# Kernel optimization log

Hardware: AMD Instinct MI355X
Metric: run time of the kernel (lower is better)

The kernel has to match this reference:

```python
import jax, jax.numpy as jnp
import numpy as np

B, S, D, H = 64, 32, 1024, 1024


def setup_inputs() -> dict:
    key = jax.random.key(0)
    ks = jax.random.split(key, 12)
    sd = 1.0 / np.sqrt(D)
    sh = 1.0 / np.sqrt(H)
    return {
        "local_descs_t": jax.random.normal(ks[0], (B, S, D), jnp.float32),
        "local_descs_rot": jax.random.normal(ks[1], (B, S, D), jnp.float32),
        "scene_w": jax.random.normal(ks[2], (2 * D,), jnp.float32) * sd,
        "scene_b": jax.random.normal(ks[3], (1,), jnp.float32),
        "Wt1": jax.random.normal(ks[4], (S, D, H), jnp.float32) * sd,
        "bt1": jax.random.normal(ks[5], (S, H), jnp.float32) * 0.01,
        "Wt2": jax.random.normal(ks[6], (S, H, 3), jnp.float32) * sh,
        "bt2": jax.random.normal(ks[7], (S, 3), jnp.float32) * 0.01,
        "Wr1": jax.random.normal(ks[8], (S, D, H), jnp.float32) * sd,
        "br1": jax.random.normal(ks[9], (S, H), jnp.float32) * 0.01,
        "Wr2": jax.random.normal(ks[10], (S, H, 4), jnp.float32) * sh,
        "br2": jax.random.normal(ks[11], (S, 4), jnp.float32) * 0.01,
    }


def _pose_head(g, idx, W1, b1, W2, b2):
    # g: [B, D]; gather per-sample expert weights and run 2-layer MLP (GELU, exact erf as in F.gelu)
    h = jax.nn.gelu(jnp.einsum("bd,bdh->bh", g, W1[idx]) + b1[idx], approximate=False)
    return jnp.einsum("bh,bho->bo", h, W2[idx]) + b2[idx]


def reference(local_descs_t, local_descs_rot, scene_w, scene_b,
              Wt1, bt1, Wt2, bt2, Wr1, br1, Wr2, br2):
    # scene classification: Linear(2D -> 1) over concat descriptors, log-softmax over scenes
    logits = jnp.einsum("bsd,d->bs",
                        jnp.concatenate([local_descs_t, local_descs_rot], axis=2),
                        scene_w) + scene_b  # [B, S]
    scene_log_distr = jax.nn.log_softmax(logits, axis=1)
    idx = jnp.argmax(scene_log_distr, axis=1)  # top-1 scene per sample, [B]
    # select the chosen scene's descriptor (equivalent to one-hot mask * descs, summed over scenes)
    global_desc_t = jnp.take_along_axis(local_descs_t, idx[:, None, None], axis=1)[:, 0]    # [B, D]
    global_desc_rot = jnp.take_along_axis(local_descs_rot, idx[:, None, None], axis=1)[:, 0]
    # per-sample expert head dispatch (use_prior=False)
    x_t = _pose_head(global_desc_t, idx, Wt1, bt1, Wt2, bt2)      # [B, 3]
    x_rot = _pose_head(global_desc_rot, idx, Wr1, br1, Wr2, br2)  # [B, 4]
    expected_pose = jnp.concatenate([x_t, x_rot], axis=1)          # [B, 7]
    return expected_pose, scene_log_distr
```

## Files before the change

kernel.cpp:

```cpp
#include <hip/hip_runtime.h>
#include <math.h>

#define BB 64
#define SS 32
#define DD 1024
#define HH 1024
#define NG 40
#define GG 8

__device__ __forceinline__ float gelu_exact(float x) {
    return 0.5f * x * (1.0f + erff(x * 0.7071067811865476f));
}

#define WS_LOGITS 256
#define WS_GSCENE 8448
#define WS_GSAMP  8704
#define WS_PART   32768

__global__ __launch_bounds__(256) void logits_kernel(
    const float* __restrict__ descs_t, const float* __restrict__ descs_rot,
    const float* __restrict__ scene_w, float* __restrict__ logits)
{
    const int s = blockIdx.x, b = blockIdx.y;
    const int tid = threadIdx.x, lane = tid & 63, wave = tid >> 6;

    const float4* t4 = (const float4*)(descs_t  + ((size_t)b * SS + s) * DD);
    const float4* r4 = (const float4*)(descs_rot + ((size_t)b * SS + s) * DD);
    const float4* w4t = (const float4*)(scene_w);
    const float4* w4r = (const float4*)(scene_w + DD);

    float4 a = t4[tid], w = w4t[tid];
    float acc = a.x*w.x + a.y*w.y + a.z*w.z + a.w*w.w;
    float4 a2 = r4[tid], w2 = w4r[tid];
    acc += a2.x*w2.x + a2.y*w2.y + a2.z*w2.z + a2.w*w2.w;

    #pragma unroll
    for (int off = 32; off >= 1; off >>= 1) acc += __shfl_xor(acc, off, 64);

    __shared__ float red[4];
    if (lane == 0) red[wave] = acc;
    __syncthreads();
    if (tid == 0) logits[b * SS + s] = red[0] + red[1] + red[2] + red[3];
}

__global__ __launch_bounds__(64) void finalize_scene_kernel(
    const float* __restrict__ scene_b, float* __restrict__ logits,
    int* __restrict__ idx_ws, int* __restrict__ grp_scene, int* __restrict__ grp_samp,
    float* __restrict__ out)
{
    const int b = threadIdx.x;
    const float bias = scene_b[0];
    float lg[SS];
    float m = -1e30f; int am = 0;
    #pragma unroll
    for (int s = 0; s < SS; ++s) {
        lg[s] = logits[b * SS + s] + bias;
        if (lg[s] > m) { m = lg[s]; am = s; }
    }
    float sum = 0.f;
    #pragma unroll
    for (int s = 0; s < SS; ++s) sum += expf(lg[s] - m);
    const float lse = m + logf(sum);
    #pragma unroll
    for (int s = 0; s < SS; ++s) out[BB * 7 + b * SS + s] = lg[s] - lse;
    idx_ws[b] = am;

    __shared__ int sh_cnt[SS];
    __shared__ int sh_base[SS];
    __shared__ int sh_scene[NG];
    __shared__ int sh_samp[NG][GG];

    for (int i = b; i < NG; i += 64) sh_scene[i] = -1;
    for (int i = b; i < NG * GG; i += 64) ((int*)sh_samp)[i] = -1;

    int rank = 0;
    for (int s = 0; s < SS; ++s) {
        unsigned long long mk = __ballot(am == s);
        if (am == s) rank = __popcll(mk & ((1ull << b) - 1ull));
        if (b == s) sh_cnt[s] = (int)__popcll(mk);
    }
    __syncthreads();
    if (b == 0) {
        int acc = 0;
        for (int s = 0; s < SS; ++s) {
            sh_base[s] = acc;
            acc += (sh_cnt[s] + GG - 1) / GG;
        }
    }
    __syncthreads();
    {
        const int g = sh_base[am] + rank / GG;
        const int slot = rank % GG;
        sh_samp[g][slot] = b;
        if (slot == 0) sh_scene[g] = am;
    }
    __syncthreads();
    for (int i = b; i < NG; i += 64) grp_scene[i] = sh_scene[i];
    for (int i = b; i < NG * GG; i += 64) grp_samp[i] = ((int*)sh_samp)[i];
}

template<int DSPL>
__global__ __launch_bounds__(256) void layer1_kernel(
    const float* __restrict__ descs_t, const float* __restrict__ descs_rot,
    const float* __restrict__ Wt1, const float* __restrict__ Wr1,
    const int* __restrict__ grp_scene, const int* __restrict__ grp_samp,
    float* __restrict__ part)
{
    constexpr int DS = DD / DSPL;
    const int dsp  = blockIdx.x;
    const int g    = blockIdx.y;
    const int head = blockIdx.z;
    const int tid  = threadIdx.x;

    const int s = grp_scene[g];
    if (s < 0) return;

    __shared__ int   sh_b[GG];
    __shared__ float sh_g[DS][GG];
    if (tid < GG) sh_b[tid] = grp_samp[g * GG + tid];
    __syncthreads();

    const float* descs = head ? descs_rot : descs_t;
    for (int t = tid; t < GG * (DS / 4); t += 256) {
        const int p = t / (DS / 4);
        const int c = t % (DS / 4);
        const int b = sh_b[p];
        float4 v = make_float4(0.f, 0.f, 0.f, 0.f);
        if (b >= 0)
            v = ((const float4*)(descs + ((size_t)b * SS + s) * DD + dsp * DS))[c];
        sh_g[c * 4 + 0][p] = v.x;
        sh_g[c * 4 + 1][p] = v.y;
        sh_g[c * 4 + 2][p] = v.z;
        sh_g[c * 4 + 3][p] = v.w;
    }
    __syncthreads();

    const float* W = (head ? Wr1 : Wt1)
                   + (size_t)s * DD * HH + (size_t)dsp * DS * HH + tid * 4;

    float4 acc[GG];
    #pragma unroll
    for (int p = 0; p < GG; ++p) acc[p] = make_float4(0.f, 0.f, 0.f, 0.f);

    #pragma unroll 2
    for (int d0 = 0; d0 < DS; d0 += 4) {
        float4 w0 = *(const float4*)(W + (size_t)(d0 + 0) * HH);
        float4 w1 = *(const float4*)(W + (size_t)(d0 + 1) * HH);
        float4 w2 = *(const float4*)(W + (size_t)(d0 + 2) * HH);
        float4 w3 = *(const float4*)(W + (size_t)(d0 + 3) * HH);
        #pragma unroll
        for (int r = 0; r < 4; ++r) {
            const float4 wv = (r == 0) ? w0 : (r == 1) ? w1 : (r == 2) ? w2 : w3;
            const float4 ga = *(const float4*)&sh_g[d0 + r][0];
            const float4 gb = *(const float4*)&sh_g[d0 + r][4];
            acc[0].x += ga.x*wv.x; acc[0].y += ga.x*wv.y; acc[0].z += ga.x*wv.z; acc[0].w += ga.x*wv.w;
            acc[1].x += ga.y*wv.x; acc[1].y += ga.y*wv.y; acc[1].z += ga.y*wv.z; acc[1].w += ga.y*wv.w;
            acc[2].x += ga.z*wv.x; acc[2].y += ga.z*wv.y; acc[2].z += ga.z*wv.z; acc[2].w += ga.z*wv.w;
            acc[3].x += ga.w*wv.x; acc[3].y += ga.w*wv.y; acc[3].z += ga.w*wv.z; acc[3].w += ga.w*wv.w;
            acc[4].x += gb.x*wv.x; acc[4].y += gb.x*wv.y; acc[4].z += gb.x*wv.z; acc[4].w += gb.x*wv.w;
            acc[5].x += gb.y*wv.x; acc[5].y += gb.y*wv.y; acc[5].z += gb.y*wv.z; acc[5].w += gb.y*wv.w;
            acc[6].x += gb.z*wv.x; acc[6].y += gb.z*wv.y; acc[6].z += gb.z*wv.z; acc[6].w += gb.z*wv.w;
            acc[7].x += gb.w*wv.x; acc[7].y += gb.w*wv.y; acc[7].z += gb.w*wv.z; acc[7].w += gb.w*wv.w;
        }
    }

    #pragma unroll
    for (int p = 0; p < GG; ++p) {
        const int b = sh_b[p];
        if (b >= 0) {
            float* dst = part + (((size_t)(head * BB + b) * DSPL + dsp) * HH) + tid * 4;
            *(float4*)dst = acc[p];
        }
    }
}

template<int DSPL>
__global__ __launch_bounds__(256) void head_out_kernel(
    const float* __restrict__ bt1, const float* __restrict__ Wt2, const float* __restrict__ bt2,
    const float* __restrict__ br1, const float* __restrict__ Wr2, const float* __restrict__ br2,
    const int* __restrict__ idx_ws, const float* __restrict__ part,
    float* __restrict__ out)
{
    const int b   = blockIdx.x;
    const int tid = threadIdx.x;
    const int s   = idx_ws[b];

    __shared__ float sh_h[2][HH];
    __shared__ float sh_red[7][4];

    #pragma unroll
    for (int head = 0; head < 2; ++head) {
        const float* b1 = (head ? br1 : bt1) + (size_t)s * HH;
        const float* p0 = part + ((size_t)(head * BB + b) * DSPL) * HH;
        const int j = tid * 4;
        float4 a = *(const float4*)(p0 + j);
        #pragma unroll 8
        for (int dsp = 1; dsp < DSPL; ++dsp) {
            float4 q = *(const float4*)(p0 + (size_t)dsp * HH + j);
            a.x += q.x; a.y += q.y; a.z += q.z; a.w += q.w;
        }
        float4 bb = *(const float4*)(b1 + j);
        sh_h[head][j + 0] = gelu_exact(a.x + bb.x);
        sh_h[head][j + 1] = gelu_exact(a.y + bb.y);
        sh_h[head][j + 2] = gelu_exact(a.z + bb.z);
        sh_h[head][j + 3] = gelu_exact(a.w + bb.w);
    }
    __syncthreads();

    const float* wt2 = Wt2 + (size_t)s * HH * 3;
    const float* wr2 = Wr2 + (size_t)s * HH * 4;
    float pa[7] = {0.f, 0.f, 0.f, 0.f, 0.f, 0.f, 0.f};
    for (int j = tid; j < HH; j += 256) {
        float ht = sh_h[0][j];
        float hr = sh_h[1][j];
        pa[0] += ht * wt2[j * 3 + 0];
        pa[1] += ht * wt2[j * 3 + 1];
        pa[2] += ht * wt2[j * 3 + 2];
        pa[3] += hr * wr2[j * 4 + 0];
        pa[4] += hr * wr2[j * 4 + 1];
        pa[5] += hr * wr2[j * 4 + 2];
        pa[6] += hr * wr2[j * 4 + 3];
    }
    const int lane = tid & 63, wave = tid >> 6;
    #pragma unroll
    for (int o = 0; o < 7; ++o) {
        float v = pa[o];
        #pragma unroll
        for (int off = 32; off >= 1; off >>= 1) v += __shfl_xor(v, off, 64);
        if (lane == 0) sh_red[o][wave] = v;
    }
    __syncthreads();
    if (tid < 7) {
        float v = sh_red[tid][0] + sh_red[tid][1] + sh_red[tid][2] + sh_red[tid][3];
        float bias = (tid < 3) ? bt2[(size_t)s * 3 + tid] : br2[(size_t)s * 4 + (tid - 3)];
        out[b * 7 + tid] = v + bias;
    }
}

template<int DSPL>
static void launch_pipeline(const float* descs_t, const float* descs_rot,
                            const float* Wt1, const float* Wr1,
                            const float* bt1, const float* Wt2, const float* bt2,
                            const float* br1, const float* Wr2, const float* br2,
                            int* idx_ws, int* grp_scene, int* grp_samp, float* part,
                            float* out, hipStream_t stream) {
    layer1_kernel<DSPL><<<dim3(DSPL, NG, 2), dim3(256), 0, stream>>>(
        descs_t, descs_rot, Wt1, Wr1, grp_scene, grp_samp, part);
    head_out_kernel<DSPL><<<dim3(BB), dim3(256), 0, stream>>>(
        bt1, Wt2, bt2, br1, Wr2, br2, idx_ws, part, out);
}

extern "C" void kernel_launch(void* const* d_in, const int* in_sizes, int n_in,
                              void* d_out, int out_size, void* d_ws, size_t ws_size,
                              hipStream_t stream) {
    const float* descs_t   = (const float*)d_in[0];
    const float* descs_rot = (const float*)d_in[1];
    const float* scene_w   = (const float*)d_in[2];
    const float* scene_b   = (const float*)d_in[3];
    const float* Wt1 = (const float*)d_in[4];
    const float* bt1 = (const float*)d_in[5];
    const float* Wt2 = (const float*)d_in[6];
    const float* bt2 = (const float*)d_in[7];
    const float* Wr1 = (const float*)d_in[8];
    const float* br1 = (const float*)d_in[9];
    const float* Wr2 = (const float*)d_in[10];
    const float* br2 = (const float*)d_in[11];
    float* out = (float*)d_out;

    int*   idx_ws    = (int*)d_ws;
    float* logits    = (float*)((char*)d_ws + WS_LOGITS);
    int*   grp_scene = (int*)((char*)d_ws + WS_GSCENE);
    int*   grp_samp  = (int*)((char*)d_ws + WS_GSAMP);
    float* part      = (float*)((char*)d_ws + WS_PART);

    logits_kernel<<<dim3(SS, BB), dim3(256), 0, stream>>>(
        descs_t, descs_rot, scene_w, logits);
    finalize_scene_kernel<<<dim3(1), dim3(64), 0, stream>>>(
        scene_b, logits, idx_ws, grp_scene, grp_samp, out);

    const size_t need32 = (size_t)WS_PART + (size_t)2 * BB * 32 * HH * sizeof(float);
    const size_t need16 = (size_t)WS_PART + (size_t)2 * BB * 16 * HH * sizeof(float);
    const size_t need8  = (size_t)WS_PART + (size_t)2 * BB * 8  * HH * sizeof(float);
    if (ws_size >= need32) {
        launch_pipeline<32>(descs_t, descs_rot, Wt1, Wr1, bt1, Wt2, bt2, br1, Wr2, br2,
                            idx_ws, grp_scene, grp_samp, part, out, stream);
    } else if (ws_size >= need16) {
        launch_pipeline<16>(descs_t, descs_rot, Wt1, Wr1, bt1, Wt2, bt2, br1, Wr2, br2,
                            idx_ws, grp_scene, grp_samp, part, out, stream);
    } else if (ws_size >= need8) {
        launch_pipeline<8>(descs_t, descs_rot, Wt1, Wr1, bt1, Wt2, bt2, br1, Wr2, br2,
                            idx_ws, grp_scene, grp_samp, part, out, stream);
    } else {
        launch_pipeline<4>(descs_t, descs_rot, Wt1, Wr1, bt1, Wt2, bt2, br1, Wr2, br2,
                            idx_ws, grp_scene, grp_samp, part, out, stream);
    }
}
```

Before: 66.60 us.

## Double-buffer layer1 weight tiles into LDS via async global_load_lds

Replaces the direct per-thread global float4 weight loads in layer1 with asynchronous global-to-LDS copies (global_load_lds, 16 bytes), double-buffered across 4-row chunks so the next chunk is fetched while the current one is computed. It also drops the 32-way D split, so the pipeline now uses at most 16 splits, giving each block a longer loop and a smaller partials buffer. This adds 32 KB of LDS per block and a barrier every chunk, which may lower occupancy and add sync overhead.

```diff
diff --git a/kernel.cpp b/kernel.cpp
--- a/kernel.cpp
+++ b/kernel.cpp
@@ -10,6 +10,12 @@
 
 __device__ __forceinline__ float gelu_exact(float x) {
     return 0.5f * x * (1.0f + erff(x * 0.7071067811865476f));
+}
+
+__device__ __forceinline__ void gload_lds16(const float* g, float* l) {
+    typedef const __attribute__((address_space(1))) unsigned int GU;
+    typedef __attribute__((address_space(3))) unsigned int LU;
+    __builtin_amdgcn_global_load_lds((GU*)g, (LU*)l, 16, 0, 0);
 }
 
 #define WS_LOGITS 256
@@ -106,17 +112,21 @@
     const int* __restrict__ grp_scene, const int* __restrict__ grp_samp,
     float* __restrict__ part)
 {
-    constexpr int DS = DD / DSPL;
+    constexpr int DS  = DD / DSPL;
+    constexpr int NCH = DS / 4;
     const int dsp  = blockIdx.x;
     const int g    = blockIdx.y;
     const int head = blockIdx.z;
     const int tid  = threadIdx.x;
+    const int wave = tid >> 6, lane = tid & 63;
 
     const int s = grp_scene[g];
     if (s < 0) return;
 
     __shared__ int   sh_b[GG];
     __shared__ float sh_g[DS][GG];
+    __shared__ float sh_w[2 * 4 * HH];
+
     if (tid < GG) sh_b[tid] = grp_samp[g * GG + tid];
     __syncthreads();
 
@@ -133,24 +143,34 @@
         sh_g[c * 4 + 2][p] = v.z;
         sh_g[c * 4 + 3][p] = v.w;
     }
-    __syncthreads();
-
-    const float* W = (head ? Wr1 : Wt1)
-                   + (size_t)s * DD * HH + (size_t)dsp * DS * HH + tid * 4;
+
+    const float* W0 = (head ? Wr1 : Wt1)
+                    + (size_t)s * DD * HH + (size_t)dsp * DS * HH;
+
+    #define L1_STAGE(c, buf)                                                  \
+        _Pragma("unroll")                                                     \
+        for (int i = 0; i < 4; ++i) {                                         \
+            const int k = wave * 4 + i;                                       \
+            gload_lds16(W0 + (size_t)((c) * 4 + (k >> 2)) * HH                \
+                           + (k & 3) * 256 + lane * 4,                        \
+                        sh_w + (buf) * (4 * HH) + k * 256);                   \
+        }
 
     float4 acc[GG];
     #pragma unroll
     for (int p = 0; p < GG; ++p) acc[p] = make_float4(0.f, 0.f, 0.f, 0.f);
 
-    #pragma unroll 2
-    for (int d0 = 0; d0 < DS; d0 += 4) {
-        float4 w0 = *(const float4*)(W + (size_t)(d0 + 0) * HH);
-        float4 w1 = *(const float4*)(W + (size_t)(d0 + 1) * HH);
-        float4 w2 = *(const float4*)(W + (size_t)(d0 + 2) * HH);
-        float4 w3 = *(const float4*)(W + (size_t)(d0 + 3) * HH);
+    L1_STAGE(0, 0);
+    __syncthreads();
+
+    int cur = 0;
+    for (int c = 0; c < NCH; ++c) {
+        if (c + 1 < NCH) { L1_STAGE(c + 1, cur ^ 1); }
+        const float* wb = sh_w + cur * (4 * HH);
+        const int d0 = c * 4;
         #pragma unroll
         for (int r = 0; r < 4; ++r) {
-            const float4 wv = (r == 0) ? w0 : (r == 1) ? w1 : (r == 2) ? w2 : w3;
+            const float4 wv = *(const float4*)(wb + r * HH + (tid << 2));
             const float4 ga = *(const float4*)&sh_g[d0 + r][0];
             const float4 gb = *(const float4*)&sh_g[d0 + r][4];
             acc[0].x += ga.x*wv.x; acc[0].y += ga.x*wv.y; acc[0].z += ga.x*wv.z; acc[0].w += ga.x*wv.w;
@@ -162,7 +182,10 @@
             acc[6].x += gb.z*wv.x; acc[6].y += gb.z*wv.y; acc[6].z += gb.z*wv.z; acc[6].w += gb.z*wv.w;
             acc[7].x += gb.w*wv.x; acc[7].y += gb.w*wv.y; acc[7].z += gb.w*wv.z; acc[7].w += gb.w*wv.w;
         }
-    }
+        __syncthreads();
+        cur ^= 1;
+    }
+    #undef L1_STAGE
 
     #pragma unroll
     for (int p = 0; p < GG; ++p) {
@@ -278,13 +301,9 @@
     finalize_scene_kernel<<<dim3(1), dim3(64), 0, stream>>>(
         scene_b, logits, idx_ws, grp_scene, grp_samp, out);
 
-    const size_t need32 = (size_t)WS_PART + (size_t)2 * BB * 32 * HH * sizeof(float);
     const size_t need16 = (size_t)WS_PART + (size_t)2 * BB * 16 * HH * sizeof(float);
     const size_t need8  = (size_t)WS_PART + (size_t)2 * BB * 8  * HH * sizeof(float);
-    if (ws_size >= need32) {
-        launch_pipeline<32>(descs_t, descs_rot, Wt1, Wr1, bt1, Wt2, bt2, br1, Wr2, br2,
-                            idx_ws, grp_scene, grp_samp, part, out, stream);
-    } else if (ws_size >= need16) {
+    if (ws_size >= need16) {
         launch_pipeline<16>(descs_t, descs_rot, Wt1, Wr1, bt1, Wt2, bt2, br1, Wr2, br2,
                             idx_ws, grp_scene, grp_samp, part, out, stream);
     } else if (ws_size >= need8) {
```

Result: faster. 60.77 us (-8.7%).
